# Kernel tuning notes

Hardware: AMD Instinct MI355X
Metric: run time of the kernel (lower is better)

## Reference

```python
import jax, jax.numpy as jnp
import numpy as np

DIM = 1024
HEADS = 16
RADIUS = 4


def setup_inputs() -> dict:
    key = jax.random.key(0)
    ks = jax.random.split(key, 5)
    B, T, D = 4, 2048, DIM
    s = 1.0 / np.sqrt(D)
    x = jax.random.normal(ks[0], (B, T, D), dtype=jnp.float32)
    w_qkv = jax.random.uniform(ks[1], (3 * D, D), minval=-s, maxval=s, dtype=jnp.float32)
    b_qkv = jax.random.uniform(ks[2], (3 * D,), minval=-s, maxval=s, dtype=jnp.float32)
    w_proj = jax.random.uniform(ks[3], (D, D), minval=-s, maxval=s, dtype=jnp.float32)
    b_proj = jax.random.uniform(ks[4], (D,), minval=-s, maxval=s, dtype=jnp.float32)
    return {"x": x, "w_qkv": w_qkv, "b_qkv": b_qkv, "w_proj": w_proj, "b_proj": b_proj}


def reference(x, w_qkv, b_qkv, w_proj, b_proj):
    B, T, D = x.shape
    H = HEADS
    hd = D // H
    scale = hd ** -0.5
    qkv = x @ w_qkv.T + b_qkv                       # [B,T,3D]
    qkv = qkv.reshape(B, T, 3, H, hd).transpose(2, 0, 3, 1, 4)  # [3,B,H,T,hd]
    q, k, v = qkv[0], qkv[1], qkv[2]
    attn = jnp.einsum('bhqd,bhkd->bhqk', q, k) * scale  # [B,H,T,T]
    idx = jnp.arange(T)
    mask = jnp.abs(idx[None, :] - idx[:, None]) > RADIUS  # [T,T]
    attn = jnp.where(mask[None, None], -jnp.inf, attn)
    attn = jax.nn.softmax(attn, axis=-1)
    out = jnp.einsum('bhqk,bhkd->bhqd', attn, v)    # [B,H,T,hd]
    out = out.transpose(0, 2, 1, 3).reshape(B, T, D)
    return out @ w_proj.T + b_proj
```

## Files before the change

### kernel.cpp

```cpp
#include <hip/hip_runtime.h>
#include <hip/hip_bf16.h>
#include <cstdint>
#include <cstddef>
#include <type_traits>


typedef __hip_bfloat16 bf16;
typedef __attribute__((ext_vector_type(8))) short bf16x8;
typedef __attribute__((ext_vector_type(4))) float f32x4;
typedef __attribute__((ext_vector_type(8))) unsigned short u16x8;

#define BATCH  4
#define SEQ    2048
#define DIM    1024
#define NHEAD  16
#define HDIM   64
#define RADIUS 4
#define ROWS   (BATCH * SEQ)
#define KDIM   1024
#define NT     (KDIM / 64)
#define HSLICE (SEQ * HDIM)

__device__ __forceinline__ void async_copy16(const void* gptr, void* lptr) {
    __builtin_amdgcn_global_load_lds(
        (const __attribute__((address_space(1))) unsigned int*)(uintptr_t)gptr,
        (__attribute__((address_space(3))) unsigned int*)(uint32_t)(uintptr_t)lptr,
        16, 0, 0);
}

__global__ __launch_bounds__(256)
void cvt_all(const float* __restrict__ s1, bf16* __restrict__ d1, int n1,
             const float* __restrict__ s2, bf16* __restrict__ d2, int n2,
             const float* __restrict__ s3, bf16* __restrict__ d3, int n3) {
    int i = blockIdx.x * blockDim.x + threadIdx.x;
    const float* src; bf16* dst;
    if (i < n1)              { src = s1; dst = d1; }
    else if (i < n1 + n2)    { i -= n1; src = s2; dst = d2; }
    else if (i < n1+n2+n3)   { i -= n1 + n2; src = s3; dst = d3; }
    else return;
    const float4 a = ((const float4*)src)[2 * i];
    const float4 b = ((const float4*)src)[2 * i + 1];
    union { u16x8 v; __hip_bfloat16 h[8]; } o;
    o.h[0] = __float2bfloat16(a.x); o.h[1] = __float2bfloat16(a.y);
    o.h[2] = __float2bfloat16(a.z); o.h[3] = __float2bfloat16(a.w);
    o.h[4] = __float2bfloat16(b.x); o.h[5] = __float2bfloat16(b.y);
    o.h[6] = __float2bfloat16(b.z); o.h[7] = __float2bfloat16(b.w);
    ((u16x8*)dst)[i] = o.v;
}


#define BAR()        __builtin_amdgcn_s_barrier()
#define WAIT_LGKM0() asm volatile("s_waitcnt lgkmcnt(0)")

#define STAGE_A(buf_, half_, kt_) do {                                          \
    _Pragma("unroll")                                                           \
    for (int i_ = 0; i_ < 2; ++i_) {                                            \
        const int c_   = i_ * 512 + tid;                                        \
        const int row_ = (half_) * 128 + (c_ >> 3);                             \
        const int kg_  = (c_ & 7) ^ (row_ & 7);                                 \
        async_copy16(A + (size_t)(tileM + row_) * KDIM + (kt_) + kg_ * 8,       \
                     (char*)As[buf_] + ((half_) * 1024 + c_) * 16);             \
    } } while (0)

#define STAGE_B3(buf_, kt_) do {                                                \
    _Pragma("unroll")                                                           \
    for (int j_ = 0; j_ < 3; ++j_) {                                            \
        const int c_   = j_ * 512 + tid;                                        \
        const int row_ = c_ >> 3;                                               \
        const int kg_  = (c_ & 7) ^ (row_ & 7);                                 \
        async_copy16(B + (size_t)(tileN + row_) * KDIM + (kt_) + kg_ * 8,       \
                     (char*)Bs[buf_] + c_ * 16);                                \
    } } while (0)

#define LDA_Q(mh_) do {                                                         \
    _Pragma("unroll")                                                           \
    for (int ks_ = 0; ks_ < 2; ++ks_)                                           \
    _Pragma("unroll")                                                           \
    for (int mt_ = 0; mt_ < 4; ++mt_)                                           \
        aF[ks_][mt_] = *(const bf16x8*)(as_ +                                   \
            (size_t)(wm * 128 + (mh_) * 64 + mt_ * 16 + l16) * 64 +             \
            ((((ks_ << 2) | quad) ^ hh) << 3));                                 \
} while (0)

#define LDB_A() do {                                                            \
    _Pragma("unroll")                                                           \
    for (int ks_ = 0; ks_ < 2; ++ks_)                                           \
    _Pragma("unroll")                                                           \
    for (int nt_ = 0; nt_ < 2; ++nt_)                                           \
        bFA[ks_][nt_] = *(const bf16x8*)(bs_ +                                  \
            (size_t)(wn * 48 + nt_ * 16 + l16) * 64 +                           \
            ((((ks_ << 2) | quad) ^ hh) << 3));                                 \
} while (0)

#define LDB_B() do {                                                            \
    _Pragma("unroll")                                                           \
    for (int ks_ = 0; ks_ < 2; ++ks_)                                           \
        bFB[ks_] = *(const bf16x8*)(bs_ +                                       \
            (size_t)(wn * 48 + 32 + l16) * 64 +                                 \
            ((((ks_ << 2) | quad) ^ hh) << 3));                                 \
} while (0)

#define MFMA_N01(mh_) do {                                                      \
    _Pragma("unroll")                                                           \
    for (int ks_ = 0; ks_ < 2; ++ks_)                                           \
    _Pragma("unroll")                                                           \
    for (int mt_ = 0; mt_ < 4; ++mt_)                                           \
    _Pragma("unroll")                                                           \
    for (int nt_ = 0; nt_ < 2; ++nt_)                                           \
        acc[(mh_) * 4 + mt_][nt_] = __builtin_amdgcn_mfma_f32_16x16x32_bf16(    \
            aF[ks_][mt_], bFA[ks_][nt_], acc[(mh_) * 4 + mt_][nt_], 0, 0, 0);   \
} while (0)

#define MFMA_N2(mh_) do {                                                       \
    _Pragma("unroll")                                                           \
    for (int ks_ = 0; ks_ < 2; ++ks_)                                           \
    _Pragma("unroll")                                                           \
    for (int mt_ = 0; mt_ < 4; ++mt_)                                           \
        acc[(mh_) * 4 + mt_][2] = __builtin_amdgcn_mfma_f32_16x16x32_bf16(      \
            aF[ks_][mt_], bFB[ks_], acc[(mh_) * 4 + mt_][2], 0, 0, 0);          \
} while (0)

__global__ __launch_bounds__(512, 1)
void gemm_qkv_8p(const bf16* __restrict__ A, const bf16* __restrict__ B,
                 const float* __restrict__ bias, bf16* __restrict__ C) {
    __shared__ bf16 As[2][256 * 64];
    __shared__ bf16 Bs[2][192 * 64];

    const int tid  = threadIdx.x;
    const int l16  = tid & 15;
    const int quad = (tid >> 4) & 3;
    const int wave = tid >> 6;
    const int wm   = wave >> 2;
    const int wn   = wave & 3;
    const int hh   = l16 & 7;

    const int bid = (int)blockIdx.x;
    const int seq = (bid & 7) * 64 + (bid >> 3);
    const int tileM = (seq >> 4) * 256;
    const int tileN = (seq & 15) * 192;

    f32x4  acc[8][3] = {};
    bf16x8 aF[2][4], bFA[2][2], bFB[2];

    STAGE_A(0, 0, 0);  STAGE_A(0, 1, 0);  STAGE_B3(0, 0);
    STAGE_A(1, 0, 64); STAGE_A(1, 1, 64); STAGE_B3(1, 64);
    asm volatile("s_waitcnt vmcnt(7)" ::: "memory");
    BAR();

    #pragma unroll 1
    for (int t = 0; t < NT; ++t) {
        const int buf = t & 1;
        const bf16* __restrict__ as_ = &As[buf][0];
        const bf16* __restrict__ bs_ = &Bs[buf][0];
        const int  kt2 = (t + 2) * 64;
        const bool pf  = (t + 2 < NT);

        LDA_Q(0);
        LDB_A();
        asm volatile("s_waitcnt lgkmcnt(8)");
        BAR();
        WAIT_LGKM0();
        __builtin_amdgcn_s_setprio(1);
        MFMA_N01(0);
        __builtin_amdgcn_s_setprio(0);
        BAR();

        LDB_B();
        BAR();
        WAIT_LGKM0();
        __builtin_amdgcn_s_setprio(1);
        MFMA_N2(0);
        __builtin_amdgcn_s_setprio(0);
        BAR();

        LDA_Q(1);
        if (pf) STAGE_B3(buf, kt2);
        BAR();
        WAIT_LGKM0();
        __builtin_amdgcn_s_setprio(1);
        MFMA_N2(1);
        __builtin_amdgcn_s_setprio(0);
        BAR();

        if (pf) { STAGE_A(buf, 0, kt2); STAGE_A(buf, 1, kt2); }
        BAR();
        __builtin_amdgcn_s_setprio(1);
        MFMA_N01(1);
        __builtin_amdgcn_s_setprio(0);
        if (pf)                 asm volatile("s_waitcnt vmcnt(7)" ::: "memory");
        else if (t + 1 < NT)    asm volatile("s_waitcnt vmcnt(0)" ::: "memory");
        BAR();
    }

    float  bvs[3];
    size_t cbase[3];
    #pragma unroll
    for (int an = 0; an < 3; ++an) {
        const int cl = tileN + wn * 48 + an * 16 + l16;
        bvs[an] = bias[cl];
        const int s = cl >> 10;
        const int h = (cl >> 6) & (NHEAD - 1);
        const int d = cl & 63;
        cbase[an] = (size_t)(h * 3 + s) * HSLICE + d;
    }
    #pragma unroll
    for (int am = 0; am < 8; ++am) {
        #pragma unroll
        for (int r = 0; r < 4; ++r) {
            const int rowg = tileM + wm * 128 + am * 16 + quad * 4 + r;
            const int b  = rowg >> 11;
            const int tt = rowg & (SEQ - 1);
            const size_t rb = (size_t)b * (NHEAD * 3) * HSLICE + (size_t)tt * HDIM;
            #pragma unroll
            for (int an = 0; an < 3; ++an)
                C[rb + cbase[an]] = __float2bfloat16(acc[am][an][r] + bvs[an]);
        }
    }
}

template <int NMAT, typename OutT>
__device__ __forceinline__
void gemm_body(const bf16* __restrict__ A, const bf16* __restrict__ B,
               const float* __restrict__ bias, OutT* __restrict__ C) {
    __shared__ bf16 As[128 * 64];
    __shared__ bf16 Bs[128 * 64];

    const int tid  = threadIdx.x;
    const int lane = tid & 63;
    const int wave = tid >> 6;
    const int quad = lane >> 4;
    const int l16  = lane & 15;

    const int tileM = blockIdx.y * 128;
    const int tileN = blockIdx.x * 128;
    const int wm = (wave >> 1) * 64;
    const int wn = (wave & 1) * 64;

    f32x4 acc[4][4] = {};

    for (int kt = 0; kt < KDIM; kt += 64) {
        #pragma unroll
        for (int i = 0; i < 4; ++i) {
            const int c   = i * 256 + tid;
            const int row = c >> 3;
            const int kg  = (c & 7) ^ (row & 7);
            async_copy16(A + (size_t)(tileM + row) * KDIM + kt + kg * 8,
                         (char*)As + c * 16);
            async_copy16(B + (size_t)(tileN + row) * KDIM + kt + kg * 8,
                         (char*)Bs + c * 16);
        }
        __syncthreads();

        #pragma unroll
        for (int ks = 0; ks < 2; ++ks) {
            const int kq = ks * 4 + quad;
            const int so = (kq ^ (l16 & 7)) * 8;
            bf16x8 aF[4], bF[4];
            #pragma unroll
            for (int mt = 0; mt < 4; ++mt)
                aF[mt] = *(const bf16x8*)(As + (wm + mt * 16 + l16) * 64 + so);
            #pragma unroll
            for (int nt = 0; nt < 4; ++nt)
                bF[nt] = *(const bf16x8*)(Bs + (wn + nt * 16 + l16) * 64 + so);

            #pragma unroll
            for (int mt = 0; mt < 4; ++mt)
                #pragma unroll
                for (int nt = 0; nt < 4; ++nt)
                    acc[mt][nt] = __builtin_amdgcn_mfma_f32_16x16x32_bf16(
                        aF[mt], bF[nt], acc[mt][nt], 0, 0, 0);
        }
        __syncthreads();
    }

    #pragma unroll
    for (int nt = 0; nt < 4; ++nt) {
        const int scol = tileN + wn + nt * 16;
        const float bv = bias[scol + l16];
        #pragma unroll
        for (int mt = 0; mt < 4; ++mt) {
            #pragma unroll
            for (int r = 0; r < 4; ++r) {
                const int rowg = tileM + wm + mt * 16 + quad * 4 + r;
                const float v = acc[mt][nt][r] + bv;
                C[(size_t)rowg * NMAT + scol + l16] = v;
            }
        }
    }
}

__global__ __launch_bounds__(256)
void gemm_proj(const bf16* __restrict__ A, const bf16* __restrict__ B,
               const float* __restrict__ bias, float* __restrict__ C) {
    gemm_body<1024, float>(A, B, bias, C);
}

__device__ __forceinline__ void bf8_to_f32(const uint4 u, float* f) {
    union { uint32_t u; float f; } c;
    c.u = u.x << 16;         f[0] = c.f;
    c.u = u.x & 0xffff0000u; f[1] = c.f;
    c.u = u.y << 16;         f[2] = c.f;
    c.u = u.y & 0xffff0000u; f[3] = c.f;
    c.u = u.z << 16;         f[4] = c.f;
    c.u = u.z & 0xffff0000u; f[5] = c.f;
    c.u = u.w << 16;         f[6] = c.f;
    c.u = u.w & 0xffff0000u; f[7] = c.f;
}

__global__ __launch_bounds__(256)
void attn_banded4(const bf16* __restrict__ qkv, bf16* __restrict__ aout) {
    const int tid = threadIdx.x;
    const int qi  = tid >> 2;
    const int ch  = tid & 3;
    const int t   = blockIdx.x * 64 + qi;
    const int h   = blockIdx.y;
    const int b   = blockIdx.z;

    const size_t bh3 = (size_t)(b * NHEAD + h) * 3;
    const bf16* qb = qkv + (bh3 + 0) * HSLICE + (size_t)t * HDIM + ch * 16;
    const bf16* kb = qkv + (bh3 + 1) * HSLICE + ch * 16;
    const bf16* vb = qkv + (bh3 + 2) * HSLICE + ch * 16;
    const float scale = 0.125f;

    float q16[16];
    {
        const uint4* qp = (const uint4*)qb;
        uint4 u0 = qp[0], u1 = qp[1];
        bf8_to_f32(u0, q16); bf8_to_f32(u1, q16 + 8);
    }

    float sc[2 * RADIUS + 1];
    #pragma unroll
    for (int j = 0; j < 2 * RADIUS + 1; ++j) {
        const int k = t - RADIUS + j;
        const bool valid = (k >= 0) && (k < SEQ);
        const int kc = valid ? k : t;
        const uint4* kp = (const uint4*)(kb + (size_t)kc * HDIM);
        float kf[16];
        uint4 u0 = kp[0], u1 = kp[1];
        bf8_to_f32(u0, kf); bf8_to_f32(u1, kf + 8);
        float p = 0.f;
        #pragma unroll
        for (int e = 0; e < 16; ++e) p = fmaf(q16[e], kf[e], p);
        p += __shfl_xor(p, 1, 64);
        p += __shfl_xor(p, 2, 64);
        sc[j] = valid ? p * scale : -1e30f;
    }

    float mx = sc[0];
    #pragma unroll
    for (int j = 1; j < 2 * RADIUS + 1; ++j) mx = fmaxf(mx, sc[j]);
    float sum = 0.f;
    #pragma unroll
    for (int j = 0; j < 2 * RADIUS + 1; ++j) { sc[j] = __expf(sc[j] - mx); sum += sc[j]; }
    const float inv = 1.0f / sum;

    float o16[16];
    #pragma unroll
    for (int e = 0; e < 16; ++e) o16[e] = 0.f;
    #pragma unroll
    for (int j = 0; j < 2 * RADIUS + 1; ++j) {
        const int k = t - RADIUS + j;
        const int kc = (k >= 0 && k < SEQ) ? k : t;
        const uint4* vp = (const uint4*)(vb + (size_t)kc * HDIM);
        float vf[16];
        uint4 u0 = vp[0], u1 = vp[1];
        bf8_to_f32(u0, vf); bf8_to_f32(u1, vf + 8);
        const float w = sc[j];
        #pragma unroll
        for (int e = 0; e < 16; ++e) o16[e] = fmaf(w, vf[e], o16[e]);
    }

    bf16* op = aout + ((size_t)b * SEQ + t) * DIM + h * HDIM + ch * 16;
    #pragma unroll
    for (int c2 = 0; c2 < 2; ++c2) {
        union { u16x8 v; __hip_bfloat16 hh[8]; } o;
        #pragma unroll
        for (int e = 0; e < 8; ++e) o.hh[e] = __float2bfloat16(o16[c2 * 8 + e] * inv);
        ((u16x8*)op)[c2] = o.v;
    }
}

extern "C" void kernel_launch(void* const* d_in, const int* in_sizes, int n_in,
                              void* d_out, int out_size, void* d_ws, size_t ws_size,
                              hipStream_t stream) {
    const float* x      = (const float*)d_in[0];
    const float* w_qkv  = (const float*)d_in[1];
    const float* b_qkv  = (const float*)d_in[2];
    const float* w_proj = (const float*)d_in[3];
    const float* b_proj = (const float*)d_in[4];
    float* out = (float*)d_out;

    bf16* xb     = (bf16*)d_ws;
    bf16* wqkvb  = xb + (size_t)ROWS * DIM;
    bf16* wprojb = wqkvb + (size_t)3072 * 1024;
    bf16* qkvb   = wprojb + (size_t)1024 * 1024;
    bf16* attnb  = qkvb + (size_t)ROWS * 3072;

    const int n1 = ROWS * DIM / 8, n2 = 3072 * 1024 / 8, n3 = 1024 * 1024 / 8;
    cvt_all<<<(n1 + n2 + n3 + 255) / 256, 256, 0, stream>>>(x, xb, n1, w_qkv, wqkvb, n2,
                                                            w_proj, wprojb, n3);

    gemm_qkv_8p<<<dim3(512), 512, 0, stream>>>(xb, wqkvb, b_qkv, qkvb);

    attn_banded4<<<dim3(SEQ / 64, NHEAD, BATCH), 256, 0, stream>>>(qkvb, attnb);

    gemm_proj<<<dim3(1024 / 128, ROWS / 128), 256, 0, stream>>>(attnb, wprojb, b_proj, out);
}
```

Measured before the change: 199.0 us.

## Halve QKV GEMM M-tile to 128 rows and allow multiple blocks per CU

The QKV projection GEMM tile shrinks from 256x192 to 128x192, so the grid doubles to 1024 blocks and launch bounds allow several blocks per CU. The per-iteration schedule drops from four MFMA phases to two, with the B prefetch for the next k-step and the A prefetch two steps ahead issued inside those phases. The goal is more concurrent waves per CU to hide memory latency, at the cost of less operand reuse per block and more global traffic for the B weights.

```diff
diff --git a/kernel.cpp b/kernel.cpp
--- a/kernel.cpp
+++ b/kernel.cpp
@@ -52,14 +52,14 @@
 #define BAR()        __builtin_amdgcn_s_barrier()
 #define WAIT_LGKM0() asm volatile("s_waitcnt lgkmcnt(0)")
 
-#define STAGE_A(buf_, half_, kt_) do {                                          \
+#define STAGE_A2(buf_, kt_) do {                                                \
     _Pragma("unroll")                                                           \
     for (int i_ = 0; i_ < 2; ++i_) {                                            \
         const int c_   = i_ * 512 + tid;                                        \
-        const int row_ = (half_) * 128 + (c_ >> 3);                             \
+        const int row_ = c_ >> 3;                                               \
         const int kg_  = (c_ & 7) ^ (row_ & 7);                                 \
         async_copy16(A + (size_t)(tileM + row_) * KDIM + (kt_) + kg_ * 8,       \
-                     (char*)As[buf_] + ((half_) * 1024 + c_) * 16);             \
+                     (char*)As[buf_] + c_ * 16);                                \
     } } while (0)
 
 #define STAGE_B3(buf_, kt_) do {                                                \
@@ -72,17 +72,17 @@
                      (char*)Bs[buf_] + c_ * 16);                                \
     } } while (0)
 
-#define LDA_Q(mh_) do {                                                         \
+#define LDA8() do {                                                             \
     _Pragma("unroll")                                                           \
     for (int ks_ = 0; ks_ < 2; ++ks_)                                           \
     _Pragma("unroll")                                                           \
     for (int mt_ = 0; mt_ < 4; ++mt_)                                           \
         aF[ks_][mt_] = *(const bf16x8*)(as_ +                                   \
-            (size_t)(wm * 128 + (mh_) * 64 + mt_ * 16 + l16) * 64 +             \
+            (size_t)(wm * 64 + mt_ * 16 + l16) * 64 +                           \
             ((((ks_ << 2) | quad) ^ hh) << 3));                                 \
 } while (0)
 
-#define LDB_A() do {                                                            \
+#define LDBA() do {                                                             \
     _Pragma("unroll")                                                           \
     for (int ks_ = 0; ks_ < 2; ++ks_)                                           \
     _Pragma("unroll")                                                           \
@@ -92,7 +92,7 @@
             ((((ks_ << 2) | quad) ^ hh) << 3));                                 \
 } while (0)
 
-#define LDB_B() do {                                                            \
+#define LDBB() do {                                                             \
     _Pragma("unroll")                                                           \
     for (int ks_ = 0; ks_ < 2; ++ks_)                                           \
         bFB[ks_] = *(const bf16x8*)(bs_ +                                       \
@@ -100,30 +100,30 @@
             ((((ks_ << 2) | quad) ^ hh) << 3));                                 \
 } while (0)
 
-#define MFMA_N01(mh_) do {                                                      \
+#define MFMA_N01() do {                                                         \
     _Pragma("unroll")                                                           \
     for (int ks_ = 0; ks_ < 2; ++ks_)                                           \
     _Pragma("unroll")                                                           \
     for (int mt_ = 0; mt_ < 4; ++mt_)                                           \
     _Pragma("unroll")                                                           \
     for (int nt_ = 0; nt_ < 2; ++nt_)                                           \
-        acc[(mh_) * 4 + mt_][nt_] = __builtin_amdgcn_mfma_f32_16x16x32_bf16(    \
-            aF[ks_][mt_], bFA[ks_][nt_], acc[(mh_) * 4 + mt_][nt_], 0, 0, 0);   \
-} while (0)
-
-#define MFMA_N2(mh_) do {                                                       \
+        acc[mt_][nt_] = __builtin_amdgcn_mfma_f32_16x16x32_bf16(                \
+            aF[ks_][mt_], bFA[ks_][nt_], acc[mt_][nt_], 0, 0, 0);               \
+} while (0)
+
+#define MFMA_N2() do {                                                          \
     _Pragma("unroll")                                                           \
     for (int ks_ = 0; ks_ < 2; ++ks_)                                           \
     _Pragma("unroll")                                                           \
     for (int mt_ = 0; mt_ < 4; ++mt_)                                           \
-        acc[(mh_) * 4 + mt_][2] = __builtin_amdgcn_mfma_f32_16x16x32_bf16(      \
-            aF[ks_][mt_], bFB[ks_], acc[(mh_) * 4 + mt_][2], 0, 0, 0);          \
-} while (0)
-
-__global__ __launch_bounds__(512, 1)
-void gemm_qkv_8p(const bf16* __restrict__ A, const bf16* __restrict__ B,
+        acc[mt_][2] = __builtin_amdgcn_mfma_f32_16x16x32_bf16(                  \
+            aF[ks_][mt_], bFB[ks_], acc[mt_][2], 0, 0, 0);                      \
+} while (0)
+
+__global__ __launch_bounds__(512, 4)
+void gemm_qkv_2b(const bf16* __restrict__ A, const bf16* __restrict__ B,
                  const float* __restrict__ bias, bf16* __restrict__ C) {
-    __shared__ bf16 As[2][256 * 64];
+    __shared__ bf16 As[2][128 * 64];
     __shared__ bf16 Bs[2][192 * 64];
 
     const int tid  = threadIdx.x;
@@ -135,16 +135,15 @@
     const int hh   = l16 & 7;
 
     const int bid = (int)blockIdx.x;
-    const int seq = (bid & 7) * 64 + (bid >> 3);
-    const int tileM = (seq >> 4) * 256;
+    const int seq = (bid & 7) * 128 + (bid >> 3);
+    const int tileM = (seq >> 4) * 128;
     const int tileN = (seq & 15) * 192;
 
-    f32x4  acc[8][3] = {};
+    f32x4  acc[4][3] = {};
     bf16x8 aF[2][4], bFA[2][2], bFB[2];
 
-    STAGE_A(0, 0, 0);  STAGE_A(0, 1, 0);  STAGE_B3(0, 0);
-    STAGE_A(1, 0, 64); STAGE_A(1, 1, 64); STAGE_B3(1, 64);
-    asm volatile("s_waitcnt vmcnt(7)" ::: "memory");
+    STAGE_A2(0, 0);  STAGE_B3(0, 0);  STAGE_A2(1, 64);
+    asm volatile("s_waitcnt vmcnt(2)" ::: "memory");
     BAR();
 
     #pragma unroll 1
@@ -152,42 +151,26 @@
         const int buf = t & 1;
         const bf16* __restrict__ as_ = &As[buf][0];
         const bf16* __restrict__ bs_ = &Bs[buf][0];
-        const int  kt2 = (t + 2) * 64;
-        const bool pf  = (t + 2 < NT);
-
-        LDA_Q(0);
-        LDB_A();
+
+        LDA8();
+        LDBA();
+        if (t + 1 < NT) STAGE_B3(buf ^ 1, (t + 1) * 64);
         asm volatile("s_waitcnt lgkmcnt(8)");
         BAR();
         WAIT_LGKM0();
         __builtin_amdgcn_s_setprio(1);
-        MFMA_N01(0);
+        MFMA_N01();
         __builtin_amdgcn_s_setprio(0);
         BAR();
 
-        LDB_B();
+        LDBB();
+        if (t + 2 < NT) STAGE_A2(buf, (t + 2) * 64);
         BAR();
         WAIT_LGKM0();
         __builtin_amdgcn_s_setprio(1);
-        MFMA_N2(0);
+        MFMA_N2();
         __builtin_amdgcn_s_setprio(0);
-        BAR();
-
-        LDA_Q(1);
-        if (pf) STAGE_B3(buf, kt2);
-        BAR();
-        WAIT_LGKM0();
-        __builtin_amdgcn_s_setprio(1);
-        MFMA_N2(1);
-        __builtin_amdgcn_s_setprio(0);
-        BAR();
-
-        if (pf) { STAGE_A(buf, 0, kt2); STAGE_A(buf, 1, kt2); }
-        BAR();
-        __builtin_amdgcn_s_setprio(1);
-        MFMA_N01(1);
-        __builtin_amdgcn_s_setprio(0);
-        if (pf)                 asm volatile("s_waitcnt vmcnt(7)" ::: "memory");
+        if (t + 2 < NT)         asm volatile("s_waitcnt vmcnt(2)" ::: "memory");
         else if (t + 1 < NT)    asm volatile("s_waitcnt vmcnt(0)" ::: "memory");
         BAR();
     }
@@ -204,16 +187,16 @@
         cbase[an] = (size_t)(h * 3 + s) * HSLICE + d;
     }
     #pragma unroll
-    for (int am = 0; am < 8; ++am) {
+    for (int mt = 0; mt < 4; ++mt) {
         #pragma unroll
         for (int r = 0; r < 4; ++r) {
-            const int rowg = tileM + wm * 128 + am * 16 + quad * 4 + r;
+            const int rowg = tileM + wm * 64 + mt * 16 + quad * 4 + r;
             const int b  = rowg >> 11;
             const int tt = rowg & (SEQ - 1);
             const size_t rb = (size_t)b * (NHEAD * 3) * HSLICE + (size_t)tt * HDIM;
             #pragma unroll
             for (int an = 0; an < 3; ++an)
-                C[rb + cbase[an]] = __float2bfloat16(acc[am][an][r] + bvs[an]);
+                C[rb + cbase[an]] = __float2bfloat16(acc[mt][an][r] + bvs[an]);
         }
     }
 }
@@ -401,7 +384,7 @@
     cvt_all<<<(n1 + n2 + n3 + 255) / 256, 256, 0, stream>>>(x, xb, n1, w_qkv, wqkvb, n2,
                                                             w_proj, wprojb, n3);
 
-    gemm_qkv_8p<<<dim3(512), 512, 0, stream>>>(xb, wqkvb, b_qkv, qkvb);
+    gemm_qkv_2b<<<dim3(1024), 512, 0, stream>>>(xb, wqkvb, b_qkv, qkvb);
 
     attn_banded4<<<dim3(SEQ / 64, NHEAD, BATCH), 256, 0, stream>>>(qkvb, attnb);
 
```

After: 191.7 us. 1.04x faster.
